# Performance work log

Hardware: AMD Instinct MI355X
Metric: run time of the kernel (lower is better)

The kernel has to match this reference:

```python
import jax, jax.numpy as jnp
import numpy as np
from jax import lax

EMBED = 512
HIDDEN = 1024
VOCAB = 50257
BATCH = 64


def setup_inputs() -> dict:
    key = jax.random.key(0)
    ks = jax.random.split(key, 7)
    s_ih = 1.0 / np.sqrt(HIDDEN)
    inp = {
        "features": jax.random.normal(ks[0], (BATCH, EMBED), dtype=jnp.float32),
        "W_ih": jax.random.uniform(ks[1], (4 * HIDDEN, EMBED), jnp.float32, -s_ih, s_ih),
        "W_hh": jax.random.uniform(ks[2], (4 * HIDDEN, HIDDEN), jnp.float32, -s_ih, s_ih),
        "b_ih": jax.random.uniform(ks[3], (4 * HIDDEN,), jnp.float32, -s_ih, s_ih),
        "b_hh": jax.random.uniform(ks[4], (4 * HIDDEN,), jnp.float32, -s_ih, s_ih),
        "W_fc": jax.random.uniform(ks[5], (VOCAB, HIDDEN), jnp.float32, -s_ih, s_ih),
        "b_fc": jax.random.uniform(ks[6], (VOCAB,), jnp.float32, -s_ih, s_ih),
        "max_seq_len": 18,
    }
    return inp


def reference(features, W_ih, W_hh, b_ih, b_hh, W_fc, b_fc, max_seq_len):
    # features: [B, E] fed at EVERY step (module re-feeds the same features).
    B = features.shape[0]
    H = W_hh.shape[1]
    # Input projection is constant across steps; hoist it (same math).
    x_proj = features @ W_ih.T + b_ih  # [B, 4H]

    def step(carry, _):
        h, c = carry
        gates = x_proj + h @ W_hh.T + b_hh  # [B, 4H], PyTorch gate order i,f,g,o
        i, f, g, o = jnp.split(gates, 4, axis=1)
        i = jax.nn.sigmoid(i)
        f = jax.nn.sigmoid(f)
        g = jnp.tanh(g)
        o = jax.nn.sigmoid(o)
        c_new = f * c + i * g
        h_new = o * jnp.tanh(c_new)
        out = h_new @ W_fc.T + b_fc  # [B, V]
        return (h_new, c_new), out

    h0 = jnp.zeros((B, H), dtype=features.dtype)
    c0 = jnp.zeros((B, H), dtype=features.dtype)
    _, outs = lax.scan(step, (h0, c0), None, length=max_seq_len)  # [T, B, V]
    return jnp.transpose(outs, (1, 0, 2))  # [B, T, V]
```

## Files before the change

### kernel.cpp

```cpp
#include <hip/hip_runtime.h>

#define EMBED  512
#define HIDDEN 1024
#define G4     4096
#define VOCAB  50257
#define BATCH  64
#define TSTEPS 18
#define MROWS  (BATCH*TSTEPS)

typedef __bf16 bf16x8 __attribute__((ext_vector_type(8)));
typedef __bf16 bf16x4 __attribute__((ext_vector_type(4)));
typedef float  f32x4  __attribute__((ext_vector_type(4)));

#define WS_HA_B   0
#define WS_HB_B   131072
#define WS_C_B    262144
#define WS_XB_B   524288
#define WS_HS_B   1572864
#define WS_WHH_B  3932160

__global__ __launch_bounds__(256) void k_init(float4* ws) {
    int i = blockIdx.x * blockDim.x + threadIdx.x;
    ws[i] = make_float4(0.f, 0.f, 0.f, 0.f);
}

__global__ __launch_bounds__(256) void k_cvt(const float* __restrict__ src,
                                             __bf16* __restrict__ dst) {
    int i = (blockIdx.x * blockDim.x + threadIdx.x) * 8;
    float4 a = *(const float4*)(src + i);
    float4 b = *(const float4*)(src + i + 4);
    bf16x8 v;
    v[0] = (__bf16)a.x; v[1] = (__bf16)a.y; v[2] = (__bf16)a.z; v[3] = (__bf16)a.w;
    v[4] = (__bf16)b.x; v[5] = (__bf16)b.y; v[6] = (__bf16)b.z; v[7] = (__bf16)b.w;
    *(bf16x8*)(dst + i) = v;
}

__global__ __launch_bounds__(256) void k_xproj(const float* __restrict__ feat,
                                               const float* __restrict__ W_ih,
                                               const float* __restrict__ b_ih,
                                               const float* __restrict__ b_hh,
                                               float* __restrict__ xb) {
    __shared__ float fsh[16][EMBED];
    const int tx = threadIdx.x;
    const int rc = blockIdx.x;
    const int b0 = blockIdx.y * 16;
    {
        int row = tx >> 4, seg = tx & 15;
        const float4* src = (const float4*)(feat + (b0 + row) * EMBED + seg * 32);
        float4* dst = (float4*)(&fsh[row][seg * 32]);
        #pragma unroll
        for (int c = 0; c < 8; ++c) dst[c] = src[c];
    }
    __syncthreads();
    const int jl = tx & 15, bl = tx >> 4;
    const int r = rc * 16 + jl;
    const int b = b0 + bl;
    const float4* w  = (const float4*)(W_ih + (size_t)r * EMBED);
    const float4* h4 = (const float4*)(&fsh[bl][0]);
    float acc = 0.f;
    #pragma unroll 4
    for (int k = 0; k < EMBED / 4; ++k) {
        float4 wv = w[k], hv = h4[k];
        acc += wv.x * hv.x + wv.y * hv.y + wv.z * hv.z + wv.w * hv.w;
    }
    xb[b * G4 + r] = acc + b_ih[r] + b_hh[r];
}

#define PJT 17

__global__ __launch_bounds__(256) void k_step(const __bf16* __restrict__ h_in,
                                              __bf16* __restrict__ h_out,
                                              float* __restrict__ c,
                                              const float* __restrict__ xb,
                                              const __bf16* __restrict__ Whh,
                                              __bf16* __restrict__ hs, int t) {
    __shared__ float part[16 * 64 * PJT];
    const int tx   = threadIdx.x;
    const int wave = tx >> 6;
    const int lane = tx & 63;
    const int q    = lane >> 4;
    const int r    = lane & 15;
    const int j0   = blockIdx.x * 16;
    const int kb   = wave * 256;

    f32x4 acc[4][4];
    #pragma unroll
    for (int i = 0; i < 4; ++i)
        #pragma unroll
        for (int g = 0; g < 4; ++g)
            acc[i][g] = (f32x4){0.f, 0.f, 0.f, 0.f};

    const __bf16* aBase = h_in + (size_t)r * HIDDEN + kb + q * 8;
    const __bf16* bBase = Whh + (size_t)(j0 + r) * HIDDEN + kb + q * 8;

    #pragma unroll 2
    for (int s = 0; s < 8; ++s) {
        const int ko = s * 32;
        bf16x8 av[4], bv[4];
        #pragma unroll
        for (int i = 0; i < 4; ++i)
            av[i] = *(const bf16x8*)(aBase + (size_t)i * 16 * HIDDEN + ko);
        #pragma unroll
        for (int g = 0; g < 4; ++g)
            bv[g] = *(const bf16x8*)(bBase + (size_t)g * 1024 * HIDDEN + ko);
        #pragma unroll
        for (int i = 0; i < 4; ++i)
            #pragma unroll
            for (int g = 0; g < 4; ++g)
                acc[i][g] = __builtin_amdgcn_mfma_f32_16x16x32_bf16(av[i], bv[g], acc[i][g], 0, 0, 0);
    }

    #pragma unroll
    for (int i = 0; i < 4; ++i)
        #pragma unroll
        for (int g = 0; g < 4; ++g)
            #pragma unroll
            for (int reg = 0; reg < 4; ++reg)
                part[((wave * 4 + g) * 64 + i * 16 + q * 4 + reg) * PJT + r] = acc[i][g][reg];
    __syncthreads();

    const int jl = tx & 15;
    const int m0 = tx >> 4;
    #pragma unroll
    for (int mi = 0; mi < 4; ++mi) {
        const int m = mi * 16 + m0;
        float gsum[4];
        #pragma unroll
        for (int g = 0; g < 4; ++g) {
            float s = xb[m * G4 + g * 1024 + j0 + jl];
            #pragma unroll
            for (int w = 0; w < 4; ++w)
                s += part[((w * 4 + g) * 64 + m) * PJT + jl];
            gsum[g] = s;
        }
        const float i_ = 1.f / (1.f + expf(-gsum[0]));
        const float f_ = 1.f / (1.f + expf(-gsum[1]));
        const float g_ = tanhf(gsum[2]);
        const float o_ = 1.f / (1.f + expf(-gsum[3]));
        const int ci = m * HIDDEN + j0 + jl;
        const float cn = f_ * c[ci] + i_ * g_;
        c[ci] = cn;
        const float hn = o_ * tanhf(cn);
        const __bf16 hb = (__bf16)hn;
        h_out[ci] = hb;
        hs[(size_t)(m * TSTEPS + t) * HIDDEN + j0 + jl] = hb;
    }
}

__device__ inline bf16x8 cvt2bf8(float4 a, float4 b) {
    bf16x8 v;
    v[0] = (__bf16)a.x; v[1] = (__bf16)a.y; v[2] = (__bf16)a.z; v[3] = (__bf16)a.w;
    v[4] = (__bf16)b.x; v[5] = (__bf16)b.y; v[6] = (__bf16)b.z; v[7] = (__bf16)b.w;
    return v;
}

#define LPITCH 40
#define NBLK 393
#define MBLK 9

__global__ __launch_bounds__(256) void k_fc(const __bf16* __restrict__ hs,
                                            const float* __restrict__ W_fc,
                                            const float* __restrict__ b_fc,
                                            float* __restrict__ out) {
    __shared__ __bf16 Ash[128 * LPITCH];
    __shared__ __bf16 Bsh[128 * LPITCH];
    const int tx = threadIdx.x;
    const int bid = blockIdx.x;
    const int mb = (bid % MBLK) * 128;
    const int nb = (bid / MBLK) * 128;

    const int srow = tx >> 1;
    const int half = tx & 1;
    const __bf16* aSrc = hs + (size_t)(mb + srow) * HIDDEN + half * 16;
    const int nclamp = min(nb + srow, VOCAB - 1);
    const float4* bSrc = (const float4*)(W_fc + (size_t)nclamp * HIDDEN + half * 16);
    __bf16* aDst = &Ash[srow * LPITCH + half * 16];
    __bf16* bDst = &Bsh[srow * LPITCH + half * 16];

    const int lane = tx & 63;
    const int wave = tx >> 6;
    const int q = lane >> 4;
    const int r = lane & 15;
    const int wm = (wave >> 1) * 64;
    const int wn = (wave & 1) * 64;

    const __bf16* aF[4];
    const __bf16* bF[4];
    #pragma unroll
    for (int i = 0; i < 4; ++i) aF[i] = &Ash[(wm + i * 16 + r) * LPITCH + q * 8];
    #pragma unroll
    for (int j = 0; j < 4; ++j) bF[j] = &Bsh[(wn + j * 16 + r) * LPITCH + q * 8];

    f32x4 acc[4][4];
    #pragma unroll
    for (int i = 0; i < 4; ++i)
        #pragma unroll
        for (int j = 0; j < 4; ++j)
            acc[i][j] = (f32x4){0.f, 0.f, 0.f, 0.f};

    bf16x8 a0p = *(const bf16x8*)aSrc;
    bf16x8 a1p = *(const bf16x8*)(aSrc + 8);
    float4 f0p = bSrc[0], f1p = bSrc[1], f2p = bSrc[2], f3p = bSrc[3];
    aSrc += 32; bSrc += 8;

    for (int k0 = 0; k0 < HIDDEN; k0 += 32) {
        *(bf16x8*)aDst = a0p;
        *(bf16x8*)(aDst + 8) = a1p;
        *(bf16x8*)bDst = cvt2bf8(f0p, f1p);
        *(bf16x8*)(bDst + 8) = cvt2bf8(f2p, f3p);
        __syncthreads();
        if (k0 + 32 < HIDDEN) {
            a0p = *(const bf16x8*)aSrc;
            a1p = *(const bf16x8*)(aSrc + 8);
            f0p = bSrc[0]; f1p = bSrc[1]; f2p = bSrc[2]; f3p = bSrc[3];
            aSrc += 32; bSrc += 8;
        }
        bf16x8 av[4], bv[4];
        #pragma unroll
        for (int i = 0; i < 4; ++i) av[i] = *(const bf16x8*)aF[i];
        #pragma unroll
        for (int j = 0; j < 4; ++j) bv[j] = *(const bf16x8*)bF[j];
        #pragma unroll
        for (int i = 0; i < 4; ++i)
            #pragma unroll
            for (int j = 0; j < 4; ++j)
                acc[i][j] = __builtin_amdgcn_mfma_f32_16x16x32_bf16(av[i], bv[j], acc[i][j], 0, 0, 0);
        __syncthreads();
    }

    #pragma unroll
    for (int j = 0; j < 4; ++j) {
        const int v = nb + wn + j * 16 + r;
        if (v < VOCAB) {
            const float bias = b_fc[v];
            #pragma unroll
            for (int i = 0; i < 4; ++i) {
                const int m0 = mb + wm + i * 16 + q * 4;
                float* op = out + (size_t)m0 * VOCAB + v;
                op[0]                 = acc[i][j][0] + bias;
                op[(size_t)VOCAB]     = acc[i][j][1] + bias;
                op[(size_t)VOCAB * 2] = acc[i][j][2] + bias;
                op[(size_t)VOCAB * 3] = acc[i][j][3] + bias;
            }
        }
    }
}

extern "C" void kernel_launch(void* const* d_in, const int* in_sizes, int n_in,
                              void* d_out, int out_size, void* d_ws, size_t ws_size,
                              hipStream_t stream) {
    const float* feat = (const float*)d_in[0];
    const float* W_ih = (const float*)d_in[1];
    const float* W_hh = (const float*)d_in[2];
    const float* b_ih = (const float*)d_in[3];
    const float* b_hh = (const float*)d_in[4];
    const float* W_fc = (const float*)d_in[5];
    const float* b_fc = (const float*)d_in[6];
    float* out = (float*)d_out;

    char* wsb = (char*)d_ws;
    __bf16* hA  = (__bf16*)(wsb + WS_HA_B);
    __bf16* hB  = (__bf16*)(wsb + WS_HB_B);
    float*  c   = (float*)(wsb + WS_C_B);
    float*  xb  = (float*)(wsb + WS_XB_B);
    __bf16* hs  = (__bf16*)(wsb + WS_HS_B);
    __bf16* Whh = (__bf16*)(wsb + WS_WHH_B);

    k_init<<<128, 256, 0, stream>>>((float4*)wsb);
    k_cvt<<<2048, 256, 0, stream>>>(W_hh, Whh);
    k_xproj<<<dim3(256, 4), 256, 0, stream>>>(feat, W_ih, b_ih, b_hh, xb);
    for (int t = 0; t < TSTEPS; ++t) {
        const __bf16* hi = (t & 1) ? hB : hA;
        __bf16*       ho = (t & 1) ? hA : hB;
        k_step<<<64, 256, 0, stream>>>(hi, ho, c, xb, Whh, hs, t);
    }
    k_fc<<<NBLK * MBLK, 256, 0, stream>>>(hs, W_fc, b_fc, out);
}
```

Before: 954.2 us.

## Fuse LSTM steps into one persistent kernel with grid barrier and register-resident weights

Replaces the 18 per-step launches with a single persistent 64-block kernel that synchronises steps through a global atomic barrier, keeps the bf16 W_hh slice in registers (converted once from fp32 in-kernel), and holds c and the input projection in registers. The first step is special-cased, since h0 is zero and its matmul can be skipped, and the init and convert kernels are dropped. The FC kernel's block index is remapped so that consecutive tiles land on the same XCD for better L2 reuse. The grid barrier relies on all 64 blocks being co-resident and adds spin-wait cost.

```diff
diff --git a/kernel.cpp b/kernel.cpp
--- a/kernel.cpp
+++ b/kernel.cpp
@@ -9,37 +9,31 @@
 #define MROWS  (BATCH*TSTEPS)
 
 typedef __bf16 bf16x8 __attribute__((ext_vector_type(8)));
-typedef __bf16 bf16x4 __attribute__((ext_vector_type(4)));
 typedef float  f32x4  __attribute__((ext_vector_type(4)));
 
 #define WS_HA_B   0
 #define WS_HB_B   131072
-#define WS_C_B    262144
+#define WS_BAR_B  262144
 #define WS_XB_B   524288
 #define WS_HS_B   1572864
-#define WS_WHH_B  3932160
-
-__global__ __launch_bounds__(256) void k_init(float4* ws) {
-    int i = blockIdx.x * blockDim.x + threadIdx.x;
-    ws[i] = make_float4(0.f, 0.f, 0.f, 0.f);
-}
-
-__global__ __launch_bounds__(256) void k_cvt(const float* __restrict__ src,
-                                             __bf16* __restrict__ dst) {
-    int i = (blockIdx.x * blockDim.x + threadIdx.x) * 8;
-    float4 a = *(const float4*)(src + i);
-    float4 b = *(const float4*)(src + i + 4);
+
+#define NLSTM_BLK 64
+
+__device__ inline bf16x8 cvt2bf8(float4 a, float4 b) {
     bf16x8 v;
     v[0] = (__bf16)a.x; v[1] = (__bf16)a.y; v[2] = (__bf16)a.z; v[3] = (__bf16)a.w;
     v[4] = (__bf16)b.x; v[5] = (__bf16)b.y; v[6] = (__bf16)b.z; v[7] = (__bf16)b.w;
-    *(bf16x8*)(dst + i) = v;
+    return v;
 }
 
 __global__ __launch_bounds__(256) void k_xproj(const float* __restrict__ feat,
                                                const float* __restrict__ W_ih,
                                                const float* __restrict__ b_ih,
                                                const float* __restrict__ b_hh,
-                                               float* __restrict__ xb) {
+                                               float* __restrict__ xb,
+                                               unsigned* __restrict__ bar) {
+    if (blockIdx.x == 0 && blockIdx.y == 0 && threadIdx.x < 2)
+        bar[threadIdx.x] = 0u;
     __shared__ float fsh[16][EMBED];
     const int tx = threadIdx.x;
     const int rc = blockIdx.x;
@@ -66,14 +60,32 @@
     xb[b * G4 + r] = acc + b_ih[r] + b_hh[r];
 }
 
+__device__ __forceinline__ void grid_barrier(unsigned* bar) {
+    __syncthreads();
+    if (threadIdx.x == 0) {
+        __threadfence();
+        unsigned gen = __hip_atomic_load(&bar[1], __ATOMIC_RELAXED, __HIP_MEMORY_SCOPE_AGENT);
+        unsigned n = __hip_atomic_fetch_add(&bar[0], 1u, __ATOMIC_ACQ_REL, __HIP_MEMORY_SCOPE_AGENT);
+        if (n == NLSTM_BLK - 1u) {
+            __hip_atomic_store(&bar[0], 0u, __ATOMIC_RELAXED, __HIP_MEMORY_SCOPE_AGENT);
+            __hip_atomic_store(&bar[1], gen + 1u, __ATOMIC_RELEASE, __HIP_MEMORY_SCOPE_AGENT);
+        } else {
+            while (__hip_atomic_load(&bar[1], __ATOMIC_ACQUIRE, __HIP_MEMORY_SCOPE_AGENT) == gen)
+                __builtin_amdgcn_s_sleep(8);
+        }
+        __threadfence();
+    }
+    __syncthreads();
+}
+
 #define PJT 17
 
-__global__ __launch_bounds__(256) void k_step(const __bf16* __restrict__ h_in,
-                                              __bf16* __restrict__ h_out,
-                                              float* __restrict__ c,
-                                              const float* __restrict__ xb,
-                                              const __bf16* __restrict__ Whh,
-                                              __bf16* __restrict__ hs, int t) {
+__global__ __launch_bounds__(256, 1) void k_lstm(const float* __restrict__ xb,
+                                                 const float* __restrict__ Whh32,
+                                                 __bf16* __restrict__ hA,
+                                                 __bf16* __restrict__ hB,
+                                                 __bf16* __restrict__ hs,
+                                                 unsigned* __restrict__ bar) {
     __shared__ float part[16 * 64 * PJT];
     const int tx   = threadIdx.x;
     const int wave = tx >> 6;
@@ -83,80 +95,114 @@
     const int j0   = blockIdx.x * 16;
     const int kb   = wave * 256;
 
-    f32x4 acc[4][4];
-    #pragma unroll
-    for (int i = 0; i < 4; ++i)
+    bf16x8 bB[4][8];
+    {
+        const float* bsrc = Whh32 + (size_t)(j0 + r) * HIDDEN + kb + q * 8;
         #pragma unroll
         for (int g = 0; g < 4; ++g)
-            acc[i][g] = (f32x4){0.f, 0.f, 0.f, 0.f};
-
-    const __bf16* aBase = h_in + (size_t)r * HIDDEN + kb + q * 8;
-    const __bf16* bBase = Whh + (size_t)(j0 + r) * HIDDEN + kb + q * 8;
-
-    #pragma unroll 2
-    for (int s = 0; s < 8; ++s) {
-        const int ko = s * 32;
-        bf16x8 av[4], bv[4];
-        #pragma unroll
-        for (int i = 0; i < 4; ++i)
-            av[i] = *(const bf16x8*)(aBase + (size_t)i * 16 * HIDDEN + ko);
-        #pragma unroll
-        for (int g = 0; g < 4; ++g)
-            bv[g] = *(const bf16x8*)(bBase + (size_t)g * 1024 * HIDDEN + ko);
-        #pragma unroll
-        for (int i = 0; i < 4; ++i)
-            #pragma unroll
-            for (int g = 0; g < 4; ++g)
-                acc[i][g] = __builtin_amdgcn_mfma_f32_16x16x32_bf16(av[i], bv[g], acc[i][g], 0, 0, 0);
-    }
-
-    #pragma unroll
-    for (int i = 0; i < 4; ++i)
-        #pragma unroll
-        for (int g = 0; g < 4; ++g)
-            #pragma unroll
-            for (int reg = 0; reg < 4; ++reg)
-                part[((wave * 4 + g) * 64 + i * 16 + q * 4 + reg) * PJT + r] = acc[i][g][reg];
-    __syncthreads();
+            #pragma unroll
+            for (int s = 0; s < 8; ++s) {
+                const float4* p = (const float4*)(bsrc + (size_t)g * 1024 * HIDDEN + s * 32);
+                bB[g][s] = cvt2bf8(p[0], p[1]);
+            }
+    }
 
     const int jl = tx & 15;
     const int m0 = tx >> 4;
+    float cr[4];
+    float xbr[4][4];
+    #pragma unroll
+    for (int mi = 0; mi < 4; ++mi) {
+        cr[mi] = 0.f;
+        const int m = mi * 16 + m0;
+        #pragma unroll
+        for (int g = 0; g < 4; ++g)
+            xbr[mi][g] = xb[m * G4 + g * 1024 + j0 + jl];
+    }
+
     #pragma unroll
     for (int mi = 0; mi < 4; ++mi) {
         const int m = mi * 16 + m0;
-        float gsum[4];
-        #pragma unroll
-        for (int g = 0; g < 4; ++g) {
-            float s = xb[m * G4 + g * 1024 + j0 + jl];
-            #pragma unroll
-            for (int w = 0; w < 4; ++w)
-                s += part[((w * 4 + g) * 64 + m) * PJT + jl];
-            gsum[g] = s;
-        }
-        const float i_ = 1.f / (1.f + expf(-gsum[0]));
-        const float f_ = 1.f / (1.f + expf(-gsum[1]));
-        const float g_ = tanhf(gsum[2]);
-        const float o_ = 1.f / (1.f + expf(-gsum[3]));
-        const int ci = m * HIDDEN + j0 + jl;
-        const float cn = f_ * c[ci] + i_ * g_;
-        c[ci] = cn;
+        const float i_ = 1.f / (1.f + expf(-xbr[mi][0]));
+        const float g_ = tanhf(xbr[mi][2]);
+        const float o_ = 1.f / (1.f + expf(-xbr[mi][3]));
+        const float cn = i_ * g_;
+        cr[mi] = cn;
         const float hn = o_ * tanhf(cn);
         const __bf16 hb = (__bf16)hn;
-        h_out[ci] = hb;
-        hs[(size_t)(m * TSTEPS + t) * HIDDEN + j0 + jl] = hb;
-    }
-}
-
-__device__ inline bf16x8 cvt2bf8(float4 a, float4 b) {
-    bf16x8 v;
-    v[0] = (__bf16)a.x; v[1] = (__bf16)a.y; v[2] = (__bf16)a.z; v[3] = (__bf16)a.w;
-    v[4] = (__bf16)b.x; v[5] = (__bf16)b.y; v[6] = (__bf16)b.z; v[7] = (__bf16)b.w;
-    return v;
+        hB[m * HIDDEN + j0 + jl] = hb;
+        hs[(size_t)(m * TSTEPS + 0) * HIDDEN + j0 + jl] = hb;
+    }
+
+    #pragma unroll 1
+    for (int t = 1; t < TSTEPS; ++t) {
+        grid_barrier(bar);
+        const __bf16* hi = (t & 1) ? hB : hA;
+        __bf16*       ho = (t & 1) ? hA : hB;
+
+        f32x4 acc[4][4];
+        #pragma unroll
+        for (int i = 0; i < 4; ++i)
+            #pragma unroll
+            for (int g = 0; g < 4; ++g)
+                acc[i][g] = (f32x4){0.f, 0.f, 0.f, 0.f};
+
+        const __bf16* aBase = hi + (size_t)r * HIDDEN + kb + q * 8;
+        #pragma unroll
+        for (int s = 0; s < 8; ++s) {
+            const int ko = s * 32;
+            bf16x8 av[4];
+            #pragma unroll
+            for (int i = 0; i < 4; ++i)
+                av[i] = *(const bf16x8*)(aBase + (size_t)i * 16 * HIDDEN + ko);
+            #pragma unroll
+            for (int i = 0; i < 4; ++i)
+                #pragma unroll
+                for (int g = 0; g < 4; ++g)
+                    acc[i][g] = __builtin_amdgcn_mfma_f32_16x16x32_bf16(av[i], bB[g][s], acc[i][g], 0, 0, 0);
+        }
+
+        #pragma unroll
+        for (int i = 0; i < 4; ++i)
+            #pragma unroll
+            for (int g = 0; g < 4; ++g)
+                #pragma unroll
+                for (int reg = 0; reg < 4; ++reg)
+                    part[((wave * 4 + g) * 64 + i * 16 + q * 4 + reg) * PJT + r] = acc[i][g][reg];
+        __syncthreads();
+
+        #pragma unroll
+        for (int mi = 0; mi < 4; ++mi) {
+            const int m = mi * 16 + m0;
+            float gsum[4];
+            #pragma unroll
+            for (int g = 0; g < 4; ++g) {
+                float s = xbr[mi][g];
+                #pragma unroll
+                for (int w = 0; w < 4; ++w)
+                    s += part[((w * 4 + g) * 64 + m) * PJT + jl];
+                gsum[g] = s;
+            }
+            const float i_ = 1.f / (1.f + expf(-gsum[0]));
+            const float f_ = 1.f / (1.f + expf(-gsum[1]));
+            const float g_ = tanhf(gsum[2]);
+            const float o_ = 1.f / (1.f + expf(-gsum[3]));
+            const float cn = f_ * cr[mi] + i_ * g_;
+            cr[mi] = cn;
+            const float hn = o_ * tanhf(cn);
+            const __bf16 hb = (__bf16)hn;
+            ho[m * HIDDEN + j0 + jl] = hb;
+            hs[(size_t)(m * TSTEPS + t) * HIDDEN + j0 + jl] = hb;
+        }
+    }
 }
 
 #define LPITCH 40
 #define NBLK 393
 #define MBLK 9
+#define NWG  (NBLK*MBLK)
+#define XQ   (NWG/8)
+#define XR   (NWG%8)
 
 __global__ __launch_bounds__(256) void k_fc(const __bf16* __restrict__ hs,
                                             const float* __restrict__ W_fc,
@@ -166,8 +212,12 @@
     __shared__ __bf16 Bsh[128 * LPITCH];
     const int tx = threadIdx.x;
     const int bid = blockIdx.x;
-    const int mb = (bid % MBLK) * 128;
-    const int nb = (bid / MBLK) * 128;
+    const int xcd = bid & 7;
+    const int lid = bid >> 3;
+    const int base = (xcd < XR) ? xcd * (XQ + 1) : XR * (XQ + 1) + (xcd - XR) * XQ;
+    const int virt = base + lid;
+    const int mb = (virt % MBLK) * 128;
+    const int nb = (virt / MBLK) * 128;
 
     const int srow = tx >> 1;
     const int half = tx & 1;
@@ -259,20 +309,13 @@
     float* out = (float*)d_out;
 
     char* wsb = (char*)d_ws;
-    __bf16* hA  = (__bf16*)(wsb + WS_HA_B);
-    __bf16* hB  = (__bf16*)(wsb + WS_HB_B);
-    float*  c   = (float*)(wsb + WS_C_B);
-    float*  xb  = (float*)(wsb + WS_XB_B);
-    __bf16* hs  = (__bf16*)(wsb + WS_HS_B);
-    __bf16* Whh = (__bf16*)(wsb + WS_WHH_B);
-
-    k_init<<<128, 256, 0, stream>>>((float4*)wsb);
-    k_cvt<<<2048, 256, 0, stream>>>(W_hh, Whh);
-    k_xproj<<<dim3(256, 4), 256, 0, stream>>>(feat, W_ih, b_ih, b_hh, xb);
-    for (int t = 0; t < TSTEPS; ++t) {
-        const __bf16* hi = (t & 1) ? hB : hA;
-        __bf16*       ho = (t & 1) ? hA : hB;
-        k_step<<<64, 256, 0, stream>>>(hi, ho, c, xb, Whh, hs, t);
-    }
-    k_fc<<<NBLK * MBLK, 256, 0, stream>>>(hs, W_fc, b_fc, out);
-}
+    __bf16*   hA  = (__bf16*)(wsb + WS_HA_B);
+    __bf16*   hB  = (__bf16*)(wsb + WS_HB_B);
+    unsigned* bar = (unsigned*)(wsb + WS_BAR_B);
+    float*    xb  = (float*)(wsb + WS_XB_B);
+    __bf16*   hs  = (__bf16*)(wsb + WS_HS_B);
+
+    k_xproj<<<dim3(256, 4), 256, 0, stream>>>(feat, W_ih, b_ih, b_hh, xb, bar);
+    k_lstm<<<NLSTM_BLK, 256, 0, stream>>>(xb, W_hh, hA, hB, hs, bar);
+    k_fc<<<NWG, 256, 0, stream>>>(hs, W_fc, b_fc, out);
+}
```

After: 929.7 us. 1.03x faster.
